# Kernel optimization log

Hardware: AMD Instinct MI355X
Metric: run time of the kernel (lower is better)

The kernel has to match this reference:

```python
import jax, jax.numpy as jnp
import numpy as np

N_NODES = 50000


def setup_inputs() -> dict:
    key = jax.random.key(0)
    k1, k2, k3, k4, k5, k6 = jax.random.split(key, 6)
    N, T, F_IN, F_OUT, E = N_NODES, 4, 64, 64, 800000
    node_features = jax.random.normal(k1, (N, T, F_IN), dtype=jnp.float32)
    edge_weights = jax.random.uniform(k2, (T, E), dtype=jnp.float32)
    src = jax.random.randint(k3, (E,), 0, N, dtype=jnp.int32)
    dst = jax.random.randint(k4, (E,), 0, N, dtype=jnp.int32)
    weight = jax.random.normal(k5, (F_OUT, F_IN), dtype=jnp.float32) / np.sqrt(F_IN)
    bias = jax.random.normal(k6, (F_OUT,), dtype=jnp.float32) * 0.01
    return {"node_features": node_features, "edge_weights": edge_weights,
            "src": src, "dst": dst, "weight": weight, "bias": bias}


def reference(node_features, edge_weights, src, dst, weight, bias):
    # edge_weights: (T, E) -> per-edge weights (E, T)
    ew = edge_weights.T  # (E, T)
    # gather source node features: (E, T, F); multiply by per-edge/timestep scalar
    msg = ew[:, :, None] * node_features[src]  # (E, T, F)
    # scatter-sum into destination nodes: (N, T, F)
    h = jax.ops.segment_sum(msg, dst, num_segments=N_NODES)
    # final linear: (N, T, F_out)
    out = jnp.einsum('ntf,of->nto', h, weight) + bias
    return out
```

## Files before the change

kernel.cpp:

```cpp
#include <hip/hip_runtime.h>


#define F_DIM 64
#define TF 256

typedef __attribute__((ext_vector_type(8))) short bf16x8;
typedef __attribute__((ext_vector_type(4))) float f32x4;
union frag_u { bf16x8 v; unsigned short s[8]; };

__device__ __forceinline__ unsigned short f2bf(float x) {
  unsigned u = __float_as_uint(x);
  return (unsigned short)((u + 0x7FFF + ((u >> 16) & 1)) >> 16);
}
__device__ __forceinline__ float bf2f(unsigned short b) {
  return __uint_as_float(((unsigned)b) << 16);
}

__global__ __launch_bounds__(256) void hist_kernel(
    const int* __restrict__ dst, int* __restrict__ cnt, int E) {
  int e = blockIdx.x * 256 + threadIdx.x;
  if (e < E) atomicAdd(&cnt[dst[e]], 1);
}

__global__ __launch_bounds__(1024) void scanA_kernel(
    const int* __restrict__ cnt, int* __restrict__ off, int* __restrict__ bsum, int N) {
  __shared__ int wsum[16];
  int tid = threadIdx.x;
  int i = blockIdx.x * 1024 + tid;
  int v = (i < N) ? cnt[i] : 0;
  int lane = tid & 63;
  int incl = v;
  #pragma unroll
  for (int s = 1; s < 64; s <<= 1) {
    int t = __shfl_up(incl, s, 64);
    if (lane >= s) incl += t;
  }
  int w = tid >> 6;
  if (lane == 63) wsum[w] = incl;
  __syncthreads();
  if (w == 0) {
    int x = (lane < 16) ? wsum[lane] : 0;
    #pragma unroll
    for (int s = 1; s < 16; s <<= 1) {
      int t = __shfl_up(x, s, 64);
      if (lane >= s) x += t;
    }
    if (lane < 16) wsum[lane] = x;
  }
  __syncthreads();
  int wpre = (w == 0) ? 0 : wsum[w - 1];
  if (i < N) off[i] = wpre + incl - v;
  if (tid == 1023) bsum[blockIdx.x] = wpre + incl;
}

__global__ __launch_bounds__(64) void scanB_kernel(int* __restrict__ bsum, int nb) {
  int lane = threadIdx.x;
  int v = (lane < nb) ? bsum[lane] : 0;
  int incl = v;
  #pragma unroll
  for (int s = 1; s < 64; s <<= 1) {
    int t = __shfl_up(incl, s, 64);
    if (lane >= s) incl += t;
  }
  if (lane < nb) bsum[lane] = incl - v;
}

__global__ __launch_bounds__(256) void fill_transform_kernel(
    const int* __restrict__ dst, const int* __restrict__ src,
    const float* __restrict__ ew, const int* __restrict__ off,
    const int* __restrict__ bsum, int* __restrict__ cnt,
    uint4* __restrict__ rec, int E, int fillBlocks,
    const float4* __restrict__ nf4, const float* __restrict__ W,
    unsigned short* __restrict__ nfb, int nrows) {
  int tid = threadIdx.x;
  if ((int)blockIdx.x < fillBlocks) {
    int stride = fillBlocks * 256;
    for (int e = blockIdx.x * 256 + tid; e < E; e += stride) {
      int d = dst[e];
      int pos = off[d] + bsum[d >> 10] + atomicSub(&cnt[d], 1) - 1;
      unsigned w0 = f2bf(ew[e]),         w1 = f2bf(ew[E + e]);
      unsigned w2 = f2bf(ew[2 * E + e]), w3 = f2bf(ew[3 * E + e]);
      uint4 r;
      r.x = (unsigned)src[e];
      r.y = (w1 << 16) | w0;
      r.z = (w3 << 16) | w2;
      r.w = 0;
      rec[pos] = r;
    }
    return;
  }

  int lane = tid & 63;
  int l15 = lane & 15, lg = lane >> 4;
  int wid = (((int)blockIdx.x - fillBlocks) * 256 + tid) >> 6;
  int nw = ((gridDim.x - fillBlocks) * 256) >> 6;

  frag_u a[4][2];
  #pragma unroll
  for (int ot = 0; ot < 4; ++ot) {
    #pragma unroll
    for (int kh = 0; kh < 2; ++kh) {
      const float* wp = W + (ot * 16 + l15) * 64 + kh * 32 + lg * 8;
      float4 v0 = *reinterpret_cast<const float4*>(wp);
      float4 v1 = *reinterpret_cast<const float4*>(wp + 4);
      a[ot][kh].s[0] = f2bf(v0.x); a[ot][kh].s[1] = f2bf(v0.y);
      a[ot][kh].s[2] = f2bf(v0.z); a[ot][kh].s[3] = f2bf(v0.w);
      a[ot][kh].s[4] = f2bf(v1.x); a[ot][kh].s[5] = f2bf(v1.y);
      a[ot][kh].s[6] = f2bf(v1.z); a[ot][kh].s[7] = f2bf(v1.w);
    }
  }

  int ntiles = (nrows + 15) >> 4;
  for (int tile = wid; tile < ntiles; tile += nw) {
    int r = tile * 16 + l15;
    int rc = min(r, nrows - 1);
    const float4* bp = nf4 + (size_t)rc * 16 + lg * 2;
    float4 v0 = bp[0], v1 = bp[1];
    float4 v2 = bp[8], v3 = bp[9];
    frag_u b0, b1;
    b0.s[0] = f2bf(v0.x); b0.s[1] = f2bf(v0.y);
    b0.s[2] = f2bf(v0.z); b0.s[3] = f2bf(v0.w);
    b0.s[4] = f2bf(v1.x); b0.s[5] = f2bf(v1.y);
    b0.s[6] = f2bf(v1.z); b0.s[7] = f2bf(v1.w);
    b1.s[0] = f2bf(v2.x); b1.s[1] = f2bf(v2.y);
    b1.s[2] = f2bf(v2.z); b1.s[3] = f2bf(v2.w);
    b1.s[4] = f2bf(v3.x); b1.s[5] = f2bf(v3.y);
    b1.s[6] = f2bf(v3.z); b1.s[7] = f2bf(v3.w);

    f32x4 acc[4];
    #pragma unroll
    for (int ot = 0; ot < 4; ++ot) {
      f32x4 z = {0.f, 0.f, 0.f, 0.f};
      acc[ot] = __builtin_amdgcn_mfma_f32_16x16x32_bf16(a[ot][0].v, b0.v, z, 0, 0, 0);
      acc[ot] = __builtin_amdgcn_mfma_f32_16x16x32_bf16(a[ot][1].v, b1.v, acc[ot], 0, 0, 0);
    }
    if (r < nrows) {
      #pragma unroll
      for (int ot = 0; ot < 4; ++ot) {
        ushort4 u = make_ushort4(f2bf(acc[ot][0]), f2bf(acc[ot][1]),
                                 f2bf(acc[ot][2]), f2bf(acc[ot][3]));
        *reinterpret_cast<ushort4*>(
            &nfb[(size_t)r * F_DIM + ot * 16 + lg * 4]) = u;
      }
    }
  }
}

__global__ __launch_bounds__(256) void gather_bf16_kernel(
    const ushort4* __restrict__ nfb, const uint4* __restrict__ rec,
    const int* __restrict__ off, const int* __restrict__ bsum,
    const float4* __restrict__ bias4, float4* __restrict__ out4, int N, int E) {
  int idx = blockIdx.x * 256 + threadIdx.x;
  int n = idx >> 6;
  if (n >= N) return;
  n = __builtin_amdgcn_readfirstlane(n);
  int r = idx & 63, t = r >> 4, q = r & 15;
  int wsel = t >> 1;
  int wshift = (t & 1) << 4;
  int beg = off[n] + bsum[n >> 10];
  int end = (n + 1 < N) ? off[n + 1] + bsum[(n + 1) >> 10] : E;
  beg = __builtin_amdgcn_readfirstlane(beg);
  end = __builtin_amdgcn_readfirstlane(end);

  float4 acc = make_float4(0.f, 0.f, 0.f, 0.f);
  int p = beg;
  for (; p + 8 <= end; p += 8) {
    uint4 rr[8];
    #pragma unroll
    for (int j = 0; j < 8; ++j) rr[j] = rec[p + j];
    float w[8];
    ushort4 v[8];
    #pragma unroll
    for (int j = 0; j < 8; ++j) {
      w[j] = __uint_as_float(((wsel ? rr[j].z : rr[j].y) >> wshift) << 16);
      v[j] = nfb[(size_t)rr[j].x * 64 + t * 16 + q];
    }
    #pragma unroll
    for (int j = 0; j < 8; ++j) {
      acc.x += w[j] * bf2f(v[j].x);
      acc.y += w[j] * bf2f(v[j].y);
      acc.z += w[j] * bf2f(v[j].z);
      acc.w += w[j] * bf2f(v[j].w);
    }
  }
  for (; p + 4 <= end; p += 4) {
    uint4 rr[4];
    #pragma unroll
    for (int j = 0; j < 4; ++j) rr[j] = rec[p + j];
    #pragma unroll
    for (int j = 0; j < 4; ++j) {
      float w = __uint_as_float(((wsel ? rr[j].z : rr[j].y) >> wshift) << 16);
      ushort4 v = nfb[(size_t)rr[j].x * 64 + t * 16 + q];
      acc.x += w * bf2f(v.x); acc.y += w * bf2f(v.y);
      acc.z += w * bf2f(v.z); acc.w += w * bf2f(v.w);
    }
  }
  for (; p < end; ++p) {
    uint4 rr = rec[p];
    float w = __uint_as_float(((wsel ? rr.z : rr.y) >> wshift) << 16);
    ushort4 v = nfb[(size_t)rr.x * 64 + t * 16 + q];
    acc.x += w * bf2f(v.x); acc.y += w * bf2f(v.y);
    acc.z += w * bf2f(v.z); acc.w += w * bf2f(v.w);
  }
  float4 b = bias4[q];
  float4 res = make_float4(acc.x + b.x, acc.y + b.y, acc.z + b.z, acc.w + b.w);
  out4[(size_t)n * 64 + t * 16 + q] = res;
}

__global__ __launch_bounds__(256) void fill_kernel(
    const int* __restrict__ dst, const int* __restrict__ src,
    const float* __restrict__ ew, const int* __restrict__ off,
    const int* __restrict__ bsum, int* __restrict__ cnt,
    uint4* __restrict__ rec, int E) {
  int e = blockIdx.x * 256 + threadIdx.x;
  if (e < E) {
    int d = dst[e];
    int pos = off[d] + bsum[d >> 10] + atomicSub(&cnt[d], 1) - 1;
    unsigned w0 = f2bf(ew[e]),         w1 = f2bf(ew[E + e]);
    unsigned w2 = f2bf(ew[2 * E + e]), w3 = f2bf(ew[3 * E + e]);
    uint4 r;
    r.x = (unsigned)src[e];
    r.y = (w1 << 16) | w0;
    r.z = (w3 << 16) | w2;
    r.w = 0;
    rec[pos] = r;
  }
}

__global__ __launch_bounds__(256) void gather_f32_kernel(
    const float4* __restrict__ nf4, const uint4* __restrict__ rec,
    const int* __restrict__ off, const int* __restrict__ bsum,
    float4* __restrict__ h4, int N, int E) {
  int idx = blockIdx.x * 256 + threadIdx.x;
  int n = idx >> 6;
  if (n >= N) return;
  int r = idx & 63, t = r >> 4, q = r & 15;
  int wsel = t >> 1;
  int wshift = (t & 1) << 4;
  int beg = off[n] + bsum[n >> 10];
  int end = (n + 1 < N) ? off[n + 1] + bsum[(n + 1) >> 10] : E;
  float4 acc = make_float4(0.f, 0.f, 0.f, 0.f);
  for (int p = beg; p < end; ++p) {
    uint4 rr = rec[p];
    float w = __uint_as_float(((wsel ? rr.z : rr.y) >> wshift) << 16);
    float4 v = nf4[(size_t)rr.x * 64 + t * 16 + q];
    acc.x += w * v.x; acc.y += w * v.y; acc.z += w * v.z; acc.w += w * v.w;
  }
  h4[(size_t)n * 64 + t * 16 + q] = acc;
}

__global__ __launch_bounds__(256) void linear_kernel(
    float* __restrict__ h, const float* __restrict__ W,
    const float* __restrict__ bias, int nrows) {
  __shared__ float Wt[64 * 65];
  __shared__ float rows[4][64];
  int tid = threadIdx.x;
  for (int i = tid; i < 4096; i += 256) Wt[(i & 63) * 65 + (i >> 6)] = W[i];
  int rr = tid >> 6, o = tid & 63;
  float b = bias[o];
  int rbase = blockIdx.x * 32;
  for (int r0 = 0; r0 < 32; r0 += 4) {
    int row = rbase + r0 + rr;
    __syncthreads();
    if (row < nrows) rows[rr][o] = h[(size_t)row * F_DIM + o];
    __syncthreads();
    if (row < nrows) {
      float acc = b;
      #pragma unroll
      for (int f = 0; f < 64; ++f) acc += rows[rr][f] * Wt[f * 65 + o];
      h[(size_t)row * F_DIM + o] = acc;
    }
  }
}

extern "C" void kernel_launch(void* const* d_in, const int* in_sizes, int n_in,
                              void* d_out, int out_size, void* d_ws, size_t ws_size,
                              hipStream_t stream) {
  const float* nf   = (const float*)d_in[0];
  const float* ew   = (const float*)d_in[1];
  const int*   src  = (const int*)d_in[2];
  const int*   dst  = (const int*)d_in[3];
  const float* W    = (const float*)d_in[4];
  const float* bias = (const float*)d_in[5];
  float* out = (float*)d_out;

  int E = in_sizes[2];
  int N = out_size / TF;
  int nrows = out_size / F_DIM;
  int nfelems = nrows * F_DIM;

  char* wsb = (char*)d_ws;
  int* cnt  = (int*)wsb;
  int* off  = cnt + N;
  int* bsum = off + (N + 1);
  size_t ofs = ((size_t)(2 * N + 1 + 64) * 4 + 15) & ~(size_t)15;
  uint4* rec = (uint4*)(wsb + ofs);           ofs += (size_t)E * 16;
  ofs = (ofs + 511) & ~(size_t)511;
  unsigned short* nfb = (unsigned short*)(wsb + ofs);
  size_t need_bf16 = ofs + (size_t)nfelems * 2;
  bool use_bf16 = ws_size >= need_bf16;

  (void)hipMemsetAsync(cnt, 0, (size_t)N * sizeof(int), stream);

  int eblk = (E + 255) / 256;
  int sblk = (N + 1023) / 1024;

  hist_kernel<<<eblk, 256, 0, stream>>>(dst, cnt, E);
  scanA_kernel<<<sblk, 1024, 0, stream>>>(cnt, off, bsum, N);
  scanB_kernel<<<1, 64, 0, stream>>>(bsum, sblk);

  if (use_bf16) {
    int fillBlocks = 1024;
    int transformBlocks = 1024;
    fill_transform_kernel<<<fillBlocks + transformBlocks, 256, 0, stream>>>(
        dst, src, ew, off, bsum, cnt, rec, E, fillBlocks,
        (const float4*)nf, W, nfb, nrows);
    gather_bf16_kernel<<<(N * 64 + 255) / 256, 256, 0, stream>>>(
        (const ushort4*)nfb, rec, off, bsum, (const float4*)bias,
        (float4*)out, N, E);
  } else {
    fill_kernel<<<eblk, 256, 0, stream>>>(dst, src, ew, off, bsum, cnt, rec, E);
    gather_f32_kernel<<<(N * 64 + 255) / 256, 256, 0, stream>>>(
        (const float4*)nf, rec, off, bsum, (float4*)out, N, E);
    linear_kernel<<<(nrows + 31) / 32, 256, 0, stream>>>(out, W, bias, nrows);
  }
}
```

Baseline: 163.0 us.

## Fuse histogram into transform kernel and merge scans via last-block pattern

The per-edge histogram now runs inside the bf16 node-feature transform kernel, which is launched first. The two scan kernels become one, with the last-arriving block (found through an atomic counter) scanning the block sums. The fill step returns to its own kernel after the scan, so fill no longer shares a launch with the transform. This cuts kernel launches and overlaps the transform with the histogram, but the fill work is no longer concurrent with the transform.

Result: no change. 161.8 us (median of 2 runs) (-0.7%).

```diff
diff --git a/kernel.cpp b/kernel.cpp
--- a/kernel.cpp
+++ b/kernel.cpp
@@ -16,84 +16,14 @@
   return __uint_as_float(((unsigned)b) << 16);
 }
 
-__global__ __launch_bounds__(256) void hist_kernel(
+__global__ __launch_bounds__(256) void transform_hist_kernel(
+    const float4* __restrict__ nf4, const float* __restrict__ W,
+    unsigned short* __restrict__ nfb, int nrows,
     const int* __restrict__ dst, int* __restrict__ cnt, int E) {
-  int e = blockIdx.x * 256 + threadIdx.x;
-  if (e < E) atomicAdd(&cnt[dst[e]], 1);
-}
-
-__global__ __launch_bounds__(1024) void scanA_kernel(
-    const int* __restrict__ cnt, int* __restrict__ off, int* __restrict__ bsum, int N) {
-  __shared__ int wsum[16];
-  int tid = threadIdx.x;
-  int i = blockIdx.x * 1024 + tid;
-  int v = (i < N) ? cnt[i] : 0;
-  int lane = tid & 63;
-  int incl = v;
-  #pragma unroll
-  for (int s = 1; s < 64; s <<= 1) {
-    int t = __shfl_up(incl, s, 64);
-    if (lane >= s) incl += t;
-  }
-  int w = tid >> 6;
-  if (lane == 63) wsum[w] = incl;
-  __syncthreads();
-  if (w == 0) {
-    int x = (lane < 16) ? wsum[lane] : 0;
-    #pragma unroll
-    for (int s = 1; s < 16; s <<= 1) {
-      int t = __shfl_up(x, s, 64);
-      if (lane >= s) x += t;
-    }
-    if (lane < 16) wsum[lane] = x;
-  }
-  __syncthreads();
-  int wpre = (w == 0) ? 0 : wsum[w - 1];
-  if (i < N) off[i] = wpre + incl - v;
-  if (tid == 1023) bsum[blockIdx.x] = wpre + incl;
-}
-
-__global__ __launch_bounds__(64) void scanB_kernel(int* __restrict__ bsum, int nb) {
-  int lane = threadIdx.x;
-  int v = (lane < nb) ? bsum[lane] : 0;
-  int incl = v;
-  #pragma unroll
-  for (int s = 1; s < 64; s <<= 1) {
-    int t = __shfl_up(incl, s, 64);
-    if (lane >= s) incl += t;
-  }
-  if (lane < nb) bsum[lane] = incl - v;
-}
-
-__global__ __launch_bounds__(256) void fill_transform_kernel(
-    const int* __restrict__ dst, const int* __restrict__ src,
-    const float* __restrict__ ew, const int* __restrict__ off,
-    const int* __restrict__ bsum, int* __restrict__ cnt,
-    uint4* __restrict__ rec, int E, int fillBlocks,
-    const float4* __restrict__ nf4, const float* __restrict__ W,
-    unsigned short* __restrict__ nfb, int nrows) {
-  int tid = threadIdx.x;
-  if ((int)blockIdx.x < fillBlocks) {
-    int stride = fillBlocks * 256;
-    for (int e = blockIdx.x * 256 + tid; e < E; e += stride) {
-      int d = dst[e];
-      int pos = off[d] + bsum[d >> 10] + atomicSub(&cnt[d], 1) - 1;
-      unsigned w0 = f2bf(ew[e]),         w1 = f2bf(ew[E + e]);
-      unsigned w2 = f2bf(ew[2 * E + e]), w3 = f2bf(ew[3 * E + e]);
-      uint4 r;
-      r.x = (unsigned)src[e];
-      r.y = (w1 << 16) | w0;
-      r.z = (w3 << 16) | w2;
-      r.w = 0;
-      rec[pos] = r;
-    }
-    return;
-  }
-
-  int lane = tid & 63;
+  int lane = threadIdx.x & 63;
   int l15 = lane & 15, lg = lane >> 4;
-  int wid = (((int)blockIdx.x - fillBlocks) * 256 + tid) >> 6;
-  int nw = ((gridDim.x - fillBlocks) * 256) >> 6;
+  int wid = (blockIdx.x * 256 + threadIdx.x) >> 6;
+  int nw = (gridDim.x * 256) >> 6;
 
   frag_u a[4][2];
   #pragma unroll
@@ -144,67 +74,61 @@
       }
     }
   }
-}
-
-__global__ __launch_bounds__(256) void gather_bf16_kernel(
-    const ushort4* __restrict__ nfb, const uint4* __restrict__ rec,
-    const int* __restrict__ off, const int* __restrict__ bsum,
-    const float4* __restrict__ bias4, float4* __restrict__ out4, int N, int E) {
-  int idx = blockIdx.x * 256 + threadIdx.x;
-  int n = idx >> 6;
-  if (n >= N) return;
-  n = __builtin_amdgcn_readfirstlane(n);
-  int r = idx & 63, t = r >> 4, q = r & 15;
-  int wsel = t >> 1;
-  int wshift = (t & 1) << 4;
-  int beg = off[n] + bsum[n >> 10];
-  int end = (n + 1 < N) ? off[n + 1] + bsum[(n + 1) >> 10] : E;
-  beg = __builtin_amdgcn_readfirstlane(beg);
-  end = __builtin_amdgcn_readfirstlane(end);
-
-  float4 acc = make_float4(0.f, 0.f, 0.f, 0.f);
-  int p = beg;
-  for (; p + 8 <= end; p += 8) {
-    uint4 rr[8];
-    #pragma unroll
-    for (int j = 0; j < 8; ++j) rr[j] = rec[p + j];
-    float w[8];
-    ushort4 v[8];
-    #pragma unroll
-    for (int j = 0; j < 8; ++j) {
-      w[j] = __uint_as_float(((wsel ? rr[j].z : rr[j].y) >> wshift) << 16);
-      v[j] = nfb[(size_t)rr[j].x * 64 + t * 16 + q];
-    }
-    #pragma unroll
-    for (int j = 0; j < 8; ++j) {
-      acc.x += w[j] * bf2f(v[j].x);
-      acc.y += w[j] * bf2f(v[j].y);
-      acc.z += w[j] * bf2f(v[j].z);
-      acc.w += w[j] * bf2f(v[j].w);
-    }
-  }
-  for (; p + 4 <= end; p += 4) {
-    uint4 rr[4];
-    #pragma unroll
-    for (int j = 0; j < 4; ++j) rr[j] = rec[p + j];
-    #pragma unroll
-    for (int j = 0; j < 4; ++j) {
-      float w = __uint_as_float(((wsel ? rr[j].z : rr[j].y) >> wshift) << 16);
-      ushort4 v = nfb[(size_t)rr[j].x * 64 + t * 16 + q];
-      acc.x += w * bf2f(v.x); acc.y += w * bf2f(v.y);
-      acc.z += w * bf2f(v.z); acc.w += w * bf2f(v.w);
-    }
-  }
-  for (; p < end; ++p) {
-    uint4 rr = rec[p];
-    float w = __uint_as_float(((wsel ? rr.z : rr.y) >> wshift) << 16);
-    ushort4 v = nfb[(size_t)rr.x * 64 + t * 16 + q];
-    acc.x += w * bf2f(v.x); acc.y += w * bf2f(v.y);
-    acc.z += w * bf2f(v.z); acc.w += w * bf2f(v.w);
-  }
-  float4 b = bias4[q];
-  float4 res = make_float4(acc.x + b.x, acc.y + b.y, acc.z + b.z, acc.w + b.w);
-  out4[(size_t)n * 64 + t * 16 + q] = res;
+
+  int gtid = blockIdx.x * 256 + threadIdx.x;
+  int gsz = gridDim.x * 256;
+  for (int e = gtid; e < E; e += gsz) atomicAdd(&cnt[dst[e]], 1);
+}
+
+__global__ __launch_bounds__(1024) void scan_kernel(
+    const int* __restrict__ cnt, int* __restrict__ off, int* __restrict__ bsum,
+    int* __restrict__ sync, int N) {
+  __shared__ int wsum[16];
+  __shared__ int isLast;
+  int tid = threadIdx.x;
+  if (tid == 0) isLast = 0;
+  int i = blockIdx.x * 1024 + tid;
+  int v = (i < N) ? cnt[i] : 0;
+  int lane = tid & 63;
+  int incl = v;
+  #pragma unroll
+  for (int s = 1; s < 64; s <<= 1) {
+    int t = __shfl_up(incl, s, 64);
+    if (lane >= s) incl += t;
+  }
+  int w = tid >> 6;
+  if (lane == 63) wsum[w] = incl;
+  __syncthreads();
+  if (w == 0) {
+    int x = (lane < 16) ? wsum[lane] : 0;
+    #pragma unroll
+    for (int s = 1; s < 16; s <<= 1) {
+      int t = __shfl_up(x, s, 64);
+      if (lane >= s) x += t;
+    }
+    if (lane < 16) wsum[lane] = x;
+  }
+  __syncthreads();
+  int wpre = (w == 0) ? 0 : wsum[w - 1];
+  if (i < N) off[i] = wpre + incl - v;
+
+  if (tid == 1023) {
+    atomicExch(&bsum[blockIdx.x], wpre + incl);
+    __threadfence();
+    if (atomicAdd(sync, 1) == (int)gridDim.x - 1) isLast = 1;
+  }
+  __syncthreads();
+  if (isLast && tid < 64) {
+    int nb = gridDim.x;
+    int bv = (tid < nb) ? atomicAdd(&bsum[tid], 0) : 0;
+    int binc = bv;
+    #pragma unroll
+    for (int s = 1; s < 64; s <<= 1) {
+      int t = __shfl_up(binc, s, 64);
+      if (lane >= s) binc += t;
+    }
+    if (tid < nb) atomicExch(&bsum[tid], binc - bv);
+  }
 }
 
 __global__ __launch_bounds__(256) void fill_kernel(
@@ -225,6 +149,73 @@
     r.w = 0;
     rec[pos] = r;
   }
+}
+
+__global__ __launch_bounds__(256) void gather_bf16_kernel(
+    const ushort4* __restrict__ nfb, const uint4* __restrict__ rec,
+    const int* __restrict__ off, const int* __restrict__ bsum,
+    const float4* __restrict__ bias4, float4* __restrict__ out4, int N, int E) {
+  int idx = blockIdx.x * 256 + threadIdx.x;
+  int n = idx >> 6;
+  if (n >= N) return;
+  n = __builtin_amdgcn_readfirstlane(n);
+  int r = idx & 63, t = r >> 4, q = r & 15;
+  int wsel = t >> 1;
+  int wshift = (t & 1) << 4;
+  int beg = off[n] + bsum[n >> 10];
+  int end = (n + 1 < N) ? off[n + 1] + bsum[(n + 1) >> 10] : E;
+  beg = __builtin_amdgcn_readfirstlane(beg);
+  end = __builtin_amdgcn_readfirstlane(end);
+
+  float4 acc = make_float4(0.f, 0.f, 0.f, 0.f);
+  int p = beg;
+  for (; p + 8 <= end; p += 8) {
+    uint4 rr[8];
+    #pragma unroll
+    for (int j = 0; j < 8; ++j) rr[j] = rec[p + j];
+    float w[8];
+    ushort4 v[8];
+    #pragma unroll
+    for (int j = 0; j < 8; ++j) {
+      w[j] = __uint_as_float(((wsel ? rr[j].z : rr[j].y) >> wshift) << 16);
+      v[j] = nfb[(size_t)rr[j].x * 64 + t * 16 + q];
+    }
+    #pragma unroll
+    for (int j = 0; j < 8; ++j) {
+      acc.x += w[j] * bf2f(v[j].x);
+      acc.y += w[j] * bf2f(v[j].y);
+      acc.z += w[j] * bf2f(v[j].z);
+      acc.w += w[j] * bf2f(v[j].w);
+    }
+  }
+  for (; p + 4 <= end; p += 4) {
+    uint4 rr[4];
+    #pragma unroll
+    for (int j = 0; j < 4; ++j) rr[j] = rec[p + j];
+    #pragma unroll
+    for (int j = 0; j < 4; ++j) {
+      float w = __uint_as_float(((wsel ? rr[j].z : rr[j].y) >> wshift) << 16);
+      ushort4 v = nfb[(size_t)rr[j].x * 64 + t * 16 + q];
+      acc.x += w * bf2f(v.x); acc.y += w * bf2f(v.y);
+      acc.z += w * bf2f(v.z); acc.w += w * bf2f(v.w);
+    }
+  }
+  for (; p < end; ++p) {
+    uint4 rr = rec[p];
+    float w = __uint_as_float(((wsel ? rr.z : rr.y) >> wshift) << 16);
+    ushort4 v = nfb[(size_t)rr.x * 64 + t * 16 + q];
+    acc.x += w * bf2f(v.x); acc.y += w * bf2f(v.y);
+    acc.z += w * bf2f(v.z); acc.w += w * bf2f(v.w);
+  }
+  float4 b = bias4[q];
+  float4 res = make_float4(acc.x + b.x, acc.y + b.y, acc.z + b.z, acc.w + b.w);
+  out4[(size_t)n * 64 + t * 16 + q] = res;
+}
+
+__global__ __launch_bounds__(256) void hist_kernel(
+    const int* __restrict__ dst, int* __restrict__ cnt, int E) {
+  int e = blockIdx.x * 256 + threadIdx.x;
+  if (e < E) atomicAdd(&cnt[dst[e]], 1);
 }
 
 __global__ __launch_bounds__(256) void gather_f32_kernel(
@@ -291,34 +282,32 @@
 
   char* wsb = (char*)d_ws;
   int* cnt  = (int*)wsb;
-  int* off  = cnt + N;
+  int* sync = cnt + N;
+  int* off  = sync + 1;
   int* bsum = off + (N + 1);
-  size_t ofs = ((size_t)(2 * N + 1 + 64) * 4 + 15) & ~(size_t)15;
+  size_t ofs = ((size_t)(2 * N + 2 + 64) * 4 + 15) & ~(size_t)15;
   uint4* rec = (uint4*)(wsb + ofs);           ofs += (size_t)E * 16;
   ofs = (ofs + 511) & ~(size_t)511;
   unsigned short* nfb = (unsigned short*)(wsb + ofs);
   size_t need_bf16 = ofs + (size_t)nfelems * 2;
   bool use_bf16 = ws_size >= need_bf16;
 
-  (void)hipMemsetAsync(cnt, 0, (size_t)N * sizeof(int), stream);
+  (void)hipMemsetAsync(cnt, 0, (size_t)(N + 1) * sizeof(int), stream);
 
   int eblk = (E + 255) / 256;
   int sblk = (N + 1023) / 1024;
 
-  hist_kernel<<<eblk, 256, 0, stream>>>(dst, cnt, E);
-  scanA_kernel<<<sblk, 1024, 0, stream>>>(cnt, off, bsum, N);
-  scanB_kernel<<<1, 64, 0, stream>>>(bsum, sblk);
-
   if (use_bf16) {
-    int fillBlocks = 1024;
-    int transformBlocks = 1024;
-    fill_transform_kernel<<<fillBlocks + transformBlocks, 256, 0, stream>>>(
-        dst, src, ew, off, bsum, cnt, rec, E, fillBlocks,
-        (const float4*)nf, W, nfb, nrows);
+    transform_hist_kernel<<<1024, 256, 0, stream>>>(
+        (const float4*)nf, W, nfb, nrows, dst, cnt, E);
+    scan_kernel<<<sblk, 1024, 0, stream>>>(cnt, off, bsum, sync, N);
+    fill_kernel<<<eblk, 256, 0, stream>>>(dst, src, ew, off, bsum, cnt, rec, E);
     gather_bf16_kernel<<<(N * 64 + 255) / 256, 256, 0, stream>>>(
         (const ushort4*)nfb, rec, off, bsum, (const float4*)bias,
         (float4*)out, N, E);
   } else {
+    hist_kernel<<<eblk, 256, 0, stream>>>(dst, cnt, E);
+    scan_kernel<<<sblk, 1024, 0, stream>>>(cnt, off, bsum, sync, N);
     fill_kernel<<<eblk, 256, 0, stream>>>(dst, src, ew, off, bsum, cnt, rec, E);
     gather_f32_kernel<<<(N * 64 + 255) / 256, 256, 0, stream>>>(
         (const float4*)nf, rec, off, bsum, (float4*)out, N, E);
```
